# Kernel optimization log

Measured on AMD Instinct MI355X. Metric: run time of the kernel, lower is better.

## Reference

```python
import jax, jax.numpy as jnp
import numpy as np

B, S, D = 8, 4096, 1024

def setup_inputs() -> dict:
    key = jax.random.key(0)
    ks = jax.random.split(key, 5)
    scale = 1.0 / np.sqrt(D)
    x = jax.random.normal(ks[0], (B, S, D), dtype=jnp.float32)
    Wq = jax.random.normal(ks[1], (D, D), dtype=jnp.float32) * scale
    Wk = jax.random.normal(ks[2], (D, D), dtype=jnp.float32) * scale
    Wv = jax.random.normal(ks[3], (D, D), dtype=jnp.float32) * scale
    Wp = jax.random.normal(ks[4], (D, D), dtype=jnp.float32) * scale
    bp = jnp.zeros((D,), dtype=jnp.float32)
    return {"x": x, "Wq": Wq, "Wk": Wk, "Wv": Wv, "Wp": Wp, "bp": bp}

def reference(x, Wq, Wk, Wv, Wp, bp):
    # torch nn.Linear(no bias): y = x @ W^T
    q = jnp.einsum('bsd,ed->bse', x, Wq)
    k = jnp.einsum('bsd,ed->bse', x, Wk)
    v = jnp.einsum('bsd,ed->bse', x, Wv)
    # Linear attention (no softmax): (Q K^T) V == Q (K^T V), use associative order
    kv = jnp.einsum('bse,bsf->bef', k, v)       # [B, D, D]
    z = jnp.einsum('bse,bef->bsf', q, kv)       # [B, S, D]
    out = jnp.einsum('bsf,gf->bsg', z, Wp) + bp + x
    return out
```

## Files before the change

### kernel.cpp

```cpp
#include <hip/hip_runtime.h>
#include <hip/hip_bf16.h>


#define B_DIM 8
#define S_DIM 4096
#define D_DIM 1024
#define M_TOT (B_DIM * S_DIM)

using short8 = __attribute__((ext_vector_type(8))) short;
using f32x4  = __attribute__((ext_vector_type(4))) float;

#define TILE_M 128
#define TILE_N 128
#define TILE_K 64

__device__ __forceinline__ void g2l16(const void* g, void* l) {
  __builtin_amdgcn_global_load_lds(
      (const __attribute__((address_space(1))) unsigned int*)g,
      (__attribute__((address_space(3))) unsigned int*)l, 16, 0, 0);
}

__device__ __forceinline__ unsigned short f2b(float f) {
  __hip_bfloat16 h = __float2bfloat16(f);
  return __builtin_bit_cast(unsigned short, h);
}

template<bool FINAL>
__global__ __launch_bounds__(256, 3)
void gemm_bt(const unsigned short* __restrict__ A,
             const unsigned short* __restrict__ Bt,
             void* __restrict__ C,
             int K, int lda, int ldb, int ldc,
             long long sA, long long sB, long long sC,
             const float* __restrict__ bias,
             const float* __restrict__ resid)
{
  __shared__ __align__(16) unsigned short smem[TILE_M * TILE_K + TILE_N * TILE_K];
  unsigned short* As = smem;
  unsigned short* Bs = smem + TILE_M * TILE_K;

  const int tid  = threadIdx.x;
  const int wave = tid >> 6;
  const int lane = tid & 63;
  const int qd   = lane >> 4;
  const int ln   = lane & 15;
  const int wr   = (wave >> 1) * 64;
  const int wc   = (wave & 1) * 64;

  const int flat = blockIdx.y * gridDim.x + blockIdx.x;
  const int strp = flat & 7;
  const int t8   = flat >> 3;
  const int bx   = t8 % gridDim.x;
  const int by   = strp * (gridDim.y >> 3) + t8 / gridDim.x;

  const long long m0 = (long long)by * TILE_M;
  const long long n0 = (long long)bx * TILE_N;
  const int bz = blockIdx.z;

  const unsigned short* Ab = A  + (long long)bz * sA;
  const unsigned short* Bb = Bt + (long long)bz * sB;

  const int srow = tid >> 3;
  const int scg  = ((tid & 7) + (tid >> 3)) & 7;
  const unsigned short* pA = Ab + (m0 + srow) * lda + scg * 8;
  const unsigned short* pB = Bb + (n0 + srow) * ldb + scg * 8;
  const long long rsA = 32LL * lda, rsB = 32LL * ldb;
  unsigned short* lA = As + wave * 512;
  unsigned short* lB = Bs + wave * 512;

  int rowA[4], sA0[4], rowB[4], sB0[4];
#pragma unroll
  for (int i = 0; i < 4; ++i) {
    int ra = wr + i * 16 + ln;
    int rb = wc + i * 16 + ln;
    rowA[i] = ra * 64;  sA0[i] = (qd - ra) & 7;
    rowB[i] = rb * 64;  sB0[i] = (qd - rb) & 7;
  }

  f32x4 acc[4][4];
#pragma unroll
  for (int i = 0; i < 4; ++i)
#pragma unroll
    for (int j = 0; j < 4; ++j)
      acc[i][j] = (f32x4){0.f, 0.f, 0.f, 0.f};

  for (int k0 = 0; k0 < K; k0 += TILE_K) {
#pragma unroll
    for (int it = 0; it < 4; ++it) g2l16(pA + it * rsA, lA + it * 2048);
#pragma unroll
    for (int it = 0; it < 4; ++it) g2l16(pB + it * rsB, lB + it * 2048);
    __syncthreads();

#pragma unroll
    for (int kk = 0; kk < 2; ++kk) {
      short8 af[4], bf[4];
#pragma unroll
      for (int i = 0; i < 4; ++i)
        af[i] = *(const short8*)(As + rowA[i] + (((sA0[i] + kk * 4) & 7) << 3));
#pragma unroll
      for (int j = 0; j < 4; ++j)
        bf[j] = *(const short8*)(Bs + rowB[j] + (((sB0[j] + kk * 4) & 7) << 3));
#pragma unroll
      for (int i = 0; i < 4; ++i)
#pragma unroll
        for (int j = 0; j < 4; ++j)
          acc[i][j] = __builtin_amdgcn_mfma_f32_16x16x32_bf16(af[i], bf[j], acc[i][j], 0, 0, 0);
    }
    __syncthreads();
    pA += TILE_K; pB += TILE_K;
  }

  float* Ct = (float*)smem;
  const int fr = tid >> 3;
  const int fc = (tid & 7) * 4;
  const int hr = tid >> 4;
  const int hc = (tid & 15) * 4;

#pragma unroll
  for (int p = 0; p < 4; ++p) {
    __syncthreads();
    if ((wr >> 6) == (p >> 1)) {
      const int ibase = (p & 1) * 2;
#pragma unroll
      for (int ii = 0; ii < 2; ++ii)
#pragma unroll
        for (int j = 0; j < 4; ++j)
#pragma unroll
          for (int r = 0; r < 4; ++r)
            Ct[(ii * 16 + qd * 4 + r) * 132 + wc + j * 16 + ln] = acc[ibase + ii][j][r];
    }
    __syncthreads();

    if constexpr (FINAL) {
      float* Cf = (float*)C + (long long)bz * sC;
      const long long grow = m0 + p * 32 + fr;
#pragma unroll
      for (int s = 0; s < 4; ++s) {
        const int c = fc + s * 32;
        float4 v = *(const float4*)(Ct + fr * 132 + c);
        const float4 bb = *(const float4*)(bias + n0 + c);
        const float4 rr = *(const float4*)(resid + grow * ldc + n0 + c);
        v.x += bb.x + rr.x; v.y += bb.y + rr.y;
        v.z += bb.z + rr.z; v.w += bb.w + rr.w;
        *(float4*)(Cf + grow * ldc + n0 + c) = v;
      }
    } else {
      unsigned short* Cb = (unsigned short*)C + (long long)bz * sC;
#pragma unroll
      for (int rs = 0; rs < 2; ++rs) {
        const int row = hr + rs * 16;
        const long long grow = m0 + p * 32 + row;
#pragma unroll
        for (int s = 0; s < 2; ++s) {
          const int c = hc + s * 64;
          float4 v = *(const float4*)(Ct + row * 132 + c);
          ushort4 u;
          u.x = f2b(v.x); u.y = f2b(v.y); u.z = f2b(v.z); u.w = f2b(v.w);
          *(ushort4*)(Cb + grow * ldc + n0 + c) = u;
        }
      }
    }
  }
}

__global__ __launch_bounds__(256)
void transpose_bds(const unsigned short* __restrict__ src,
                   unsigned short* __restrict__ dst)
{
  __shared__ unsigned short tile[64][68];
  const int b  = blockIdx.z;
  const int s0 = blockIdx.x * 64;
  const int e0 = blockIdx.y * 64;
  const int tx = threadIdx.x & 15;
  const int ty = threadIdx.x >> 4;

#pragma unroll
  for (int r = 0; r < 4; ++r) {
    int s = ty * 4 + r;
    ushort4 d = *(const ushort4*)(src + ((size_t)b * S_DIM + s0 + s) * D_DIM + e0 + tx * 4);
    *(ushort4*)&tile[s][tx * 4] = d;
  }
  __syncthreads();
#pragma unroll
  for (int r = 0; r < 4; ++r) {
    int e = ty * 4 + r;
    ushort4 d;
    d.x = tile[tx * 4 + 0][e];
    d.y = tile[tx * 4 + 1][e];
    d.z = tile[tx * 4 + 2][e];
    d.w = tile[tx * 4 + 3][e];
    *(ushort4*)(dst + ((size_t)b * D_DIM + e0 + e) * S_DIM + s0 + tx * 4) = d;
  }
}

__global__ __launch_bounds__(256)
void cast_transpose_1k(const float* __restrict__ src, unsigned short* __restrict__ dst)
{
  __shared__ unsigned short tile[64][68];
  const int e0 = blockIdx.x * 64;
  const int d0 = blockIdx.y * 64;
  const int tx = threadIdx.x & 15;
  const int ty = threadIdx.x >> 4;

#pragma unroll
  for (int r = 0; r < 4; ++r) {
    int e = ty * 4 + r;
    float4 f = *(const float4*)(src + (size_t)(e0 + e) * D_DIM + d0 + tx * 4);
    ushort4 u;
    u.x = f2b(f.x); u.y = f2b(f.y); u.z = f2b(f.z); u.w = f2b(f.w);
    *(ushort4*)&tile[e][tx * 4] = u;
  }
  __syncthreads();
#pragma unroll
  for (int r = 0; r < 4; ++r) {
    int d = ty * 4 + r;
    ushort4 o;
    o.x = tile[tx * 4 + 0][d];
    o.y = tile[tx * 4 + 1][d];
    o.z = tile[tx * 4 + 2][d];
    o.w = tile[tx * 4 + 3][d];
    *(ushort4*)(dst + (size_t)(d0 + d) * D_DIM + e0 + tx * 4) = o;
  }
}

__global__ __launch_bounds__(256)
void cast_f32_bf16(const float* __restrict__ src, unsigned short* __restrict__ dst, int n4)
{
  int i = blockIdx.x * 256 + threadIdx.x;
  if (i >= n4) return;
  float4 f = ((const float4*)src)[i];
  ushort4 u;
  u.x = f2b(f.x); u.y = f2b(f.y); u.z = f2b(f.z); u.w = f2b(f.w);
  ((ushort4*)dst)[i] = u;
}

extern "C" void kernel_launch(void* const* d_in, const int* in_sizes, int n_in,
                              void* d_out, int out_size, void* d_ws, size_t ws_size,
                              hipStream_t stream) {
  const float* x  = (const float*)d_in[0];
  const float* Wq = (const float*)d_in[1];
  const float* Wk = (const float*)d_in[2];
  const float* Wv = (const float*)d_in[3];
  const float* Wp = (const float*)d_in[4];
  const float* bp = (const float*)d_in[5];
  float* out = (float*)d_out;
  char* ws = (char*)d_ws;

  unsigned short* xb   = (unsigned short*)(ws + 0);
  unsigned short* Wkb  = (unsigned short*)(ws + 67108864);
  unsigned short* Wvb  = (unsigned short*)(ws + 69206016);
  unsigned short* Wpb  = (unsigned short*)(ws + 71303168);
  unsigned short* WqTb = (unsigned short*)(ws + 73400320);
  unsigned short* xT   = (unsigned short*)(ws + 75497472);
  unsigned short* G    = (unsigned short*)(ws + 142606336);
  unsigned short* H2   = (unsigned short*)(ws + 159383552);
  unsigned short* T3   = (unsigned short*)(ws + 176160768);
  unsigned short* PT   = (unsigned short*)(ws + 192937984);
  unsigned short* zb   = (unsigned short*)(ws + 209715200);

  const long long DD = (long long)D_DIM * D_DIM;
  const long long SD = (long long)S_DIM * D_DIM;

  cast_f32_bf16<<<dim3(M_TOT * D_DIM / 4 / 256), 256, 0, stream>>>(x, xb, M_TOT * D_DIM / 4);
  cast_f32_bf16<<<dim3(D_DIM * D_DIM / 4 / 256), 256, 0, stream>>>(Wk, Wkb, D_DIM * D_DIM / 4);
  cast_f32_bf16<<<dim3(D_DIM * D_DIM / 4 / 256), 256, 0, stream>>>(Wv, Wvb, D_DIM * D_DIM / 4);
  cast_f32_bf16<<<dim3(D_DIM * D_DIM / 4 / 256), 256, 0, stream>>>(Wp, Wpb, D_DIM * D_DIM / 4);
  cast_transpose_1k<<<dim3(16, 16), 256, 0, stream>>>(Wq, WqTb);

  dim3 gt(S_DIM / 64, D_DIM / 64, B_DIM);
  transpose_bds<<<gt, 256, 0, stream>>>(xb, xT);

  dim3 g1k(D_DIM / TILE_N, D_DIM / TILE_M, B_DIM);
  gemm_bt<false><<<g1k, 256, 0, stream>>>(xT, xT, G, S_DIM, S_DIM, S_DIM, D_DIM,
                                          SD, SD, DD, nullptr, nullptr);

  gemm_bt<false><<<g1k, 256, 0, stream>>>(Wvb, G, H2, D_DIM, D_DIM, D_DIM, D_DIM,
                                          0, DD, DD, nullptr, nullptr);

  gemm_bt<false><<<g1k, 256, 0, stream>>>(H2, Wkb, T3, D_DIM, D_DIM, D_DIM, D_DIM,
                                          DD, 0, DD, nullptr, nullptr);

  gemm_bt<false><<<g1k, 256, 0, stream>>>(T3, WqTb, PT, D_DIM, D_DIM, D_DIM, D_DIM,
                                          DD, 0, DD, nullptr, nullptr);

  dim3 gz(D_DIM / TILE_N, S_DIM / TILE_M, B_DIM);
  gemm_bt<false><<<gz, 256, 0, stream>>>(xb, PT, zb, D_DIM, D_DIM, D_DIM, D_DIM,
                                         SD, DD, SD, nullptr, nullptr);

  dim3 gf(D_DIM / TILE_N, M_TOT / TILE_M, 1);
  gemm_bt<true><<<gf, 256, 0, stream>>>(zb, Wpb, out, D_DIM, D_DIM, D_DIM, D_DIM,
                                        0, 0, 0, bp, x);
  (void)in_sizes; (void)n_in; (void)out_size; (void)ws_size;
}
```

Before: 575.3 us.

## Fold output projection into per-batch DxD matrix, drop one large GEMM

Reassociates the chain so the output projection Wp is folded into a per-batch DxD matrix together with Wq, Wk and Wv. Two weight-only products (Wp·Wv and Wq^T·Wk) are precomputed once. The final S×D GEMM then applies that combined matrix straight to x and fuses in the bias and residual. This removes one full B·S×D×D GEMM and the bf16 z intermediate round trip, at the cost of two small weight GEMMs and extra bf16 rounding through the folded products.

```diff
diff --git a/kernel.cpp b/kernel.cpp
--- a/kernel.cpp
+++ b/kernel.cpp
@@ -133,13 +133,14 @@
 
     if constexpr (FINAL) {
       float* Cf = (float*)C + (long long)bz * sC;
+      const float* Rf = resid + (long long)bz * sC;
       const long long grow = m0 + p * 32 + fr;
 #pragma unroll
       for (int s = 0; s < 4; ++s) {
         const int c = fc + s * 32;
         float4 v = *(const float4*)(Ct + fr * 132 + c);
         const float4 bb = *(const float4*)(bias + n0 + c);
-        const float4 rr = *(const float4*)(resid + grow * ldc + n0 + c);
+        const float4 rr = *(const float4*)(Rf + grow * ldc + n0 + c);
         v.x += bb.x + rr.x; v.y += bb.y + rr.y;
         v.z += bb.z + rr.z; v.w += bb.w + rr.w;
         *(float4*)(Cf + grow * ldc + n0 + c) = v;
@@ -247,48 +248,48 @@
   char* ws = (char*)d_ws;
 
   unsigned short* xb   = (unsigned short*)(ws + 0);
-  unsigned short* Wkb  = (unsigned short*)(ws + 67108864);
-  unsigned short* Wvb  = (unsigned short*)(ws + 69206016);
-  unsigned short* Wpb  = (unsigned short*)(ws + 71303168);
-  unsigned short* WqTb = (unsigned short*)(ws + 73400320);
-  unsigned short* xT   = (unsigned short*)(ws + 75497472);
-  unsigned short* G    = (unsigned short*)(ws + 142606336);
-  unsigned short* H2   = (unsigned short*)(ws + 159383552);
-  unsigned short* T3   = (unsigned short*)(ws + 176160768);
-  unsigned short* PT   = (unsigned short*)(ws + 192937984);
-  unsigned short* zb   = (unsigned short*)(ws + 209715200);
+  unsigned short* Wpb  = (unsigned short*)(ws + 67108864);
+  unsigned short* WvTb = (unsigned short*)(ws + 69206016);
+  unsigned short* WqTb = (unsigned short*)(ws + 71303168);
+  unsigned short* WkTb = (unsigned short*)(ws + 73400320);
+  unsigned short* P1   = (unsigned short*)(ws + 75497472);
+  unsigned short* P2T  = (unsigned short*)(ws + 77594624);
+  unsigned short* xT   = (unsigned short*)(ws + 79691776);
+  unsigned short* G    = (unsigned short*)(ws + 146800640);
+  unsigned short* T    = (unsigned short*)(ws + 163577856);
+  unsigned short* ET   = (unsigned short*)(ws + 180355072);
 
   const long long DD = (long long)D_DIM * D_DIM;
   const long long SD = (long long)S_DIM * D_DIM;
 
   cast_f32_bf16<<<dim3(M_TOT * D_DIM / 4 / 256), 256, 0, stream>>>(x, xb, M_TOT * D_DIM / 4);
-  cast_f32_bf16<<<dim3(D_DIM * D_DIM / 4 / 256), 256, 0, stream>>>(Wk, Wkb, D_DIM * D_DIM / 4);
-  cast_f32_bf16<<<dim3(D_DIM * D_DIM / 4 / 256), 256, 0, stream>>>(Wv, Wvb, D_DIM * D_DIM / 4);
   cast_f32_bf16<<<dim3(D_DIM * D_DIM / 4 / 256), 256, 0, stream>>>(Wp, Wpb, D_DIM * D_DIM / 4);
+  cast_transpose_1k<<<dim3(16, 16), 256, 0, stream>>>(Wv, WvTb);
   cast_transpose_1k<<<dim3(16, 16), 256, 0, stream>>>(Wq, WqTb);
+  cast_transpose_1k<<<dim3(16, 16), 256, 0, stream>>>(Wk, WkTb);
 
   dim3 gt(S_DIM / 64, D_DIM / 64, B_DIM);
   transpose_bds<<<gt, 256, 0, stream>>>(xb, xT);
+
+  dim3 gw(D_DIM / TILE_N, D_DIM / TILE_M, 1);
+  gemm_bt<false><<<gw, 256, 0, stream>>>(Wpb, WvTb, P1, D_DIM, D_DIM, D_DIM, D_DIM,
+                                         0, 0, 0, nullptr, nullptr);
+
+  gemm_bt<false><<<gw, 256, 0, stream>>>(WqTb, WkTb, P2T, D_DIM, D_DIM, D_DIM, D_DIM,
+                                         0, 0, 0, nullptr, nullptr);
 
   dim3 g1k(D_DIM / TILE_N, D_DIM / TILE_M, B_DIM);
   gemm_bt<false><<<g1k, 256, 0, stream>>>(xT, xT, G, S_DIM, S_DIM, S_DIM, D_DIM,
                                           SD, SD, DD, nullptr, nullptr);
 
-  gemm_bt<false><<<g1k, 256, 0, stream>>>(Wvb, G, H2, D_DIM, D_DIM, D_DIM, D_DIM,
+  gemm_bt<false><<<g1k, 256, 0, stream>>>(P1, G, T, D_DIM, D_DIM, D_DIM, D_DIM,
                                           0, DD, DD, nullptr, nullptr);
 
-  gemm_bt<false><<<g1k, 256, 0, stream>>>(H2, Wkb, T3, D_DIM, D_DIM, D_DIM, D_DIM,
+  gemm_bt<false><<<g1k, 256, 0, stream>>>(T, P2T, ET, D_DIM, D_DIM, D_DIM, D_DIM,
                                           DD, 0, DD, nullptr, nullptr);
 
-  gemm_bt<false><<<g1k, 256, 0, stream>>>(T3, WqTb, PT, D_DIM, D_DIM, D_DIM, D_DIM,
-                                          DD, 0, DD, nullptr, nullptr);
-
-  dim3 gz(D_DIM / TILE_N, S_DIM / TILE_M, B_DIM);
-  gemm_bt<false><<<gz, 256, 0, stream>>>(xb, PT, zb, D_DIM, D_DIM, D_DIM, D_DIM,
-                                         SD, DD, SD, nullptr, nullptr);
-
-  dim3 gf(D_DIM / TILE_N, M_TOT / TILE_M, 1);
-  gemm_bt<true><<<gf, 256, 0, stream>>>(zb, Wpb, out, D_DIM, D_DIM, D_DIM, D_DIM,
-                                        0, 0, 0, bp, x);
+  dim3 gf(D_DIM / TILE_N, S_DIM / TILE_M, B_DIM);
+  gemm_bt<true><<<gf, 256, 0, stream>>>(xb, ET, out, D_DIM, D_DIM, D_DIM, D_DIM,
+                                        SD, DD, SD, bp, x);
   (void)in_sizes; (void)n_in; (void)out_size; (void)ws_size;
 }
```

Measured after the change: 520.5 us. 1.11x faster.
